# Kernel optimization log

Hardware: AMD Instinct MI355X
Metric: run time of the kernel (lower is better)

## Reference

```python
import jax, jax.numpy as jnp
import numpy as np

N_NODES = 100000
N_EDGES = 1600000
N_FEAT = 64
HIDDEN = 64
N_GRAPHS = 64
N_CLASSES = 2


def setup_inputs() -> dict:
    key = jax.random.key(0)
    ks = jax.random.split(key, 12)
    x = jax.random.normal(ks[0], (N_NODES, N_FEAT), dtype=jnp.float32)
    edge_index = jax.random.randint(ks[1], (2, N_EDGES), 0, N_NODES, dtype=jnp.int32)
    batch = jnp.sort(jax.random.randint(ks[2], (N_NODES,), 0, N_GRAPHS, dtype=jnp.int32))
    # Glorot-style init for GCNConv weights, zeros for biases (PyG default)
    def glorot(k, fan_in, fan_out):
        s = jnp.sqrt(6.0 / (fan_in + fan_out))
        return jax.random.uniform(k, (fan_in, fan_out), jnp.float32, -s, s)
    W1 = glorot(ks[3], N_FEAT, HIDDEN); b1 = jnp.zeros((HIDDEN,), jnp.float32)
    W2 = glorot(ks[4], HIDDEN, HIDDEN); b2 = jnp.zeros((HIDDEN,), jnp.float32)
    W3 = glorot(ks[5], HIDDEN, HIDDEN); b3 = jnp.zeros((HIDDEN,), jnp.float32)
    Wl = glorot(ks[6], HIDDEN, N_CLASSES); bl = jnp.zeros((N_CLASSES,), jnp.float32)
    return {"x": x, "edge_index": edge_index, "batch": batch,
            "W1": W1, "b1": b1, "W2": W2, "b2": b2, "W3": W3, "b3": b3,
            "Wl": Wl, "bl": bl}


def _gcn_conv(h, W, b, src, dst, dinv, n_nodes):
    # GCNConv with self-loops: out_i = sum_j d_i^-1/2 d_j^-1/2 (x_j W) + d_i^-1 (x_i W) + b
    h = h @ W                                   # [N, H]
    coef = (dinv[src] * dinv[dst])[:, None]     # [E, 1]
    agg = jax.ops.segment_sum(coef * h[src], dst, num_segments=n_nodes)
    return agg + (dinv * dinv)[:, None] * h + b


def reference(x, edge_index, batch, W1, b1, W2, b2, W3, b3, Wl, bl):
    src, dst = edge_index[0], edge_index[1]
    # degree of A + I (edge weight 1), shared by all three convs
    deg = jax.ops.segment_sum(jnp.ones((N_EDGES,), x.dtype), dst, num_segments=N_NODES) + 1.0
    dinv = jax.lax.rsqrt(deg)

    h = jax.nn.relu(_gcn_conv(x, W1, b1, src, dst, dinv, N_NODES))
    h = jax.nn.relu(_gcn_conv(h, W2, b2, src, dst, dinv, N_NODES))
    h = _gcn_conv(h, W3, b3, src, dst, dinv, N_NODES)

    # global_mean_pool over graph ids
    sums = jax.ops.segment_sum(h, batch, num_segments=N_GRAPHS)
    cnts = jax.ops.segment_sum(jnp.ones((N_NODES,), x.dtype), batch, num_segments=N_GRAPHS)
    pooled = sums / jnp.maximum(cnts, 1.0)[:, None]

    # dropout(p=0.5) is identity in eval mode
    return pooled @ Wl + bl
```

## Files before the change

### kernel.cpp

```cpp
#include <hip/hip_runtime.h>


#define NF 64
#define ELLW 64
#define BINSHIFT 9
#define BINW 512
#define NB 196
#define BINCAP 9216
#define LPITCH 68

typedef __attribute__((ext_vector_type(8))) _Float16 f16x8;
typedef __attribute__((ext_vector_type(4))) _Float16 f16x4;
typedef __attribute__((ext_vector_type(4))) float f32x4;

__device__ inline unsigned short f2h_u(float f) {
    return __builtin_bit_cast(unsigned short, (_Float16)f);
}
__device__ inline unsigned int pack_h2(float a, float b) {
    unsigned int ua = f2h_u(a), ub = f2h_u(b);
    return ua | (ub << 16);
}

__global__ void binA_kernel(const int* __restrict__ src, const int* __restrict__ dst,
                            int* __restrict__ binCnt, int* __restrict__ binEdges,
                            int nE, int chunk) {
    __shared__ int hist[NB];
    __shared__ int base[NB];
    int t = threadIdx.x;
    if (t < NB) hist[t] = 0;
    __syncthreads();
    int e0 = blockIdx.x * chunk;
    int e1 = min(e0 + chunk, nE);
    for (int e = e0 + t; e < e1; e += blockDim.x) {
        int b = dst[e] >> BINSHIFT;
        atomicAdd(&hist[b], 1);
    }
    __syncthreads();
    if (t < NB) {
        base[t] = atomicAdd(&binCnt[t], hist[t]);
        hist[t] = 0;
    }
    __syncthreads();
    for (int e = e0 + t; e < e1; e += blockDim.x) {
        int d = dst[e];
        int b = d >> BINSHIFT;
        int pos = base[b] + atomicAdd(&hist[b], 1);
        if (pos < BINCAP)
            binEdges[(size_t)b * BINCAP + pos] = src[e] | ((d & (BINW - 1)) << 17);
    }
}

__global__ void __launch_bounds__(512) binB_kernel(const int* __restrict__ binEdges,
                            const int* __restrict__ binCnt, int* __restrict__ cnt,
                            float* __restrict__ dinv, int* __restrict__ colELL, int n,
                            unsigned int* __restrict__ dummyA, unsigned int* __restrict__ dummyB) {
    __shared__ int lcnt[BINW];
    int t = threadIdx.x;
    int b = blockIdx.x;
    if (b == 0 && t < 32) { dummyA[t] = 0u; dummyB[t] = 0u; }
    for (int i = t; i < BINW; i += blockDim.x) lcnt[i] = 1;
    __syncthreads();
    int m = binCnt[b];
    if (m > BINCAP) m = BINCAP;
    const int* be = binEdges + (size_t)b * BINCAP;
    int nbase = b << BINSHIFT;
    for (int e = t; e < m; e += blockDim.x) {
        int v = be[e];
        int s = v & 0x1FFFF;
        int dl = v >> 17;
        int pos = atomicAdd(&lcnt[dl], 1);
        if (pos < ELLW) colELL[(size_t)(nbase + dl) * ELLW + pos] = s;
    }
    __syncthreads();
    for (int i = t; i < BINW; i += blockDim.x) {
        int node = nbase + i;
        if (node < n) {
            int c = lcnt[i];
            if (c > ELLW) c = ELLW;
            colELL[(size_t)node * ELLW + 0] = node;
            int cpad = (c + 3) & ~3;
            for (int j = c; j < cpad; ++j)
                colELL[(size_t)node * ELLW + j] = n;
            cnt[node] = c;
            dinv[node] = rsqrtf((float)c);
        }
    }
}

__global__ void prep_kernel(const float* __restrict__ W1, const float* __restrict__ W2,
                            const float* __restrict__ W3, unsigned short* __restrict__ w1h,
                            unsigned short* __restrict__ w2h, unsigned short* __restrict__ w3h) {
    int t = blockIdx.x * blockDim.x + threadIdx.x;
    if (t < NF * NF) {
        w1h[t] = f2h_u(W1[t]);
        w2h[t] = f2h_u(W2[t]);
        w3h[t] = f2h_u(W3[t]);
    }
}

__device__ __forceinline__ void gather_row_mlp8(
        const unsigned short* __restrict__ hB, const int* __restrict__ cr,
        int cl4, int fq, float acc[8]) {
    int q = 0;
    for (; q + 8 <= cl4; q += 8) {
        int s0 = cr[q], s1 = cr[q + 1], s2 = cr[q + 2], s3 = cr[q + 3];
        int s4 = cr[q + 4], s5 = cr[q + 5], s6 = cr[q + 6], s7 = cr[q + 7];
        f16x8 h0 = *(const f16x8*)(hB + (size_t)s0 * NF + fq * 8);
        f16x8 h1 = *(const f16x8*)(hB + (size_t)s1 * NF + fq * 8);
        f16x8 h2 = *(const f16x8*)(hB + (size_t)s2 * NF + fq * 8);
        f16x8 h3 = *(const f16x8*)(hB + (size_t)s3 * NF + fq * 8);
        f16x8 h4 = *(const f16x8*)(hB + (size_t)s4 * NF + fq * 8);
        f16x8 h5 = *(const f16x8*)(hB + (size_t)s5 * NF + fq * 8);
        f16x8 h6 = *(const f16x8*)(hB + (size_t)s6 * NF + fq * 8);
        f16x8 h7 = *(const f16x8*)(hB + (size_t)s7 * NF + fq * 8);
        f16x8 ttA = (h0 + h1) + (h2 + h3);
        f16x8 ttB = (h4 + h5) + (h6 + h7);
#pragma unroll
        for (int j = 0; j < 8; ++j) acc[j] += (float)ttA[j];
#pragma unroll
        for (int j = 0; j < 8; ++j) acc[j] += (float)ttB[j];
    }
    if (q + 4 <= cl4) {
        int s0 = cr[q], s1 = cr[q + 1], s2 = cr[q + 2], s3 = cr[q + 3];
        f16x8 h0 = *(const f16x8*)(hB + (size_t)s0 * NF + fq * 8);
        f16x8 h1 = *(const f16x8*)(hB + (size_t)s1 * NF + fq * 8);
        f16x8 h2 = *(const f16x8*)(hB + (size_t)s2 * NF + fq * 8);
        f16x8 h3 = *(const f16x8*)(hB + (size_t)s3 * NF + fq * 8);
        f16x8 tt = (h0 + h1) + (h2 + h3);
#pragma unroll
        for (int j = 0; j < 8; ++j) acc[j] += (float)tt[j];
    }
}

__device__ inline void load_W_frags(const unsigned short* __restrict__ Wh, int r16, int kq,
                                    f16x8 bfr[4][2]) {
#pragma unroll
    for (int nt = 0; nt < 4; ++nt)
#pragma unroll
        for (int kh = 0; kh < 2; ++kh) {
            f16x8 f;
#pragma unroll
            for (int j = 0; j < 8; ++j)
                f[j] = __builtin_bit_cast(_Float16,
                        Wh[(kh * 32 + kq * 8 + j) * NF + nt * 16 + r16]);
            bfr[nt][kh] = f;
        }
}

__global__ void __launch_bounds__(256) gemm1_mfma_kernel(const float* __restrict__ A,
                                                         const unsigned short* __restrict__ Wh,
                                                         const float* __restrict__ dinv,
                                                         unsigned short* __restrict__ outB, int n) {
    __shared__ unsigned short T[4][16 * LPITCH];
    int lane = threadIdx.x & 63;
    int r16 = lane & 15, kq = lane >> 4;
    int wv = threadIdx.x >> 6;
    int wid = blockIdx.x * 4 + wv;
    int nw = gridDim.x * 4;
    f16x8 bfr[4][2];
    load_W_frags(Wh, r16, kq, bfr);
    int ntiles = n >> 4;
    for (int t = wid; t < ntiles; t += nw) {
        int r0 = t << 4;
        const float* ar = A + (size_t)(r0 + r16) * NF + kq * 8;
        f16x8 a0, a1;
        float4 v0 = *(const float4*)(ar);
        float4 v1 = *(const float4*)(ar + 4);
        float4 v2 = *(const float4*)(ar + 32);
        float4 v3 = *(const float4*)(ar + 36);
        a0[0] = (_Float16)v0.x; a0[1] = (_Float16)v0.y;
        a0[2] = (_Float16)v0.z; a0[3] = (_Float16)v0.w;
        a0[4] = (_Float16)v1.x; a0[5] = (_Float16)v1.y;
        a0[6] = (_Float16)v1.z; a0[7] = (_Float16)v1.w;
        a1[0] = (_Float16)v2.x; a1[1] = (_Float16)v2.y;
        a1[2] = (_Float16)v2.z; a1[3] = (_Float16)v2.w;
        a1[4] = (_Float16)v3.x; a1[5] = (_Float16)v3.y;
        a1[6] = (_Float16)v3.z; a1[7] = (_Float16)v3.w;
        f32x4 acc[4];
#pragma unroll
        for (int nt = 0; nt < 4; ++nt) {
            acc[nt] = (f32x4)(0.0f);
            acc[nt] = __builtin_amdgcn_mfma_f32_16x16x32_f16(a0, bfr[nt][0], acc[nt], 0, 0, 0);
            acc[nt] = __builtin_amdgcn_mfma_f32_16x16x32_f16(a1, bfr[nt][1], acc[nt], 0, 0, 0);
        }
        float ds[4];
#pragma unroll
        for (int reg = 0; reg < 4; ++reg) ds[reg] = dinv[r0 + kq * 4 + reg];
        unsigned short* Tw = T[wv];
#pragma unroll
        for (int nt = 0; nt < 4; ++nt)
#pragma unroll
            for (int reg = 0; reg < 4; ++reg)
                Tw[(kq * 4 + reg) * LPITCH + nt * 16 + r16] = f2h_u(acc[nt][reg] * ds[reg]);
#pragma unroll
        for (int it = 0; it < 4; ++it) {
            int row = it * 4 + kq;
            uint2 v = *(const uint2*)&Tw[row * LPITCH + r16 * 4];
            *(uint2*)(outB + (size_t)(r0 + row) * NF + r16 * 4) = v;
        }
    }
}

__global__ void __launch_bounds__(256) fused_agg_gemm_kernel(
        const unsigned short* __restrict__ hB, const int* __restrict__ colELL,
        const int* __restrict__ cnt, const float* __restrict__ dinv,
        const float* __restrict__ bias, const unsigned short* __restrict__ Wh,
        unsigned short* __restrict__ outB, int n) {
    __shared__ int Icol[32 * 32];
    __shared__ int Icnt[32];
    __shared__ unsigned short Tin[2][2048];
    __shared__ unsigned short Tout[2][16 * LPITCH];
    int t = threadIdx.x;
    int lane = t & 63;
    int wv = t >> 6;
    int es = lane >> 3;
    int fq = lane & 7;
    int r16 = lane & 15, kq = lane >> 4;
    int r0 = (int)(blockIdx.x << 5);
    {
        int srow = t >> 3, sj = t & 7;
        ((int4*)Icol)[t] = *(const int4*)(colELL + (size_t)(r0 + srow) * ELLW + sj * 4);
    }
    if (t < 32) Icnt[t] = cnt[r0 + t];
    int s0 = (wv & 1) << 1;
    f16x8 bfr[2][2];
#pragma unroll
    for (int si = 0; si < 2; ++si)
#pragma unroll
        for (int kh = 0; kh < 2; ++kh) {
            f16x8 f;
#pragma unroll
            for (int j = 0; j < 8; ++j)
                f[j] = __builtin_bit_cast(_Float16,
                        Wh[(kh * 32 + kq * 8 + j) * NF + (s0 + si) * 16 + r16]);
            bfr[si][kh] = f;
        }
    __syncthreads();
    int lrow = wv * 8 + es;
    int row = r0 + lrow;
    int c = Icnt[lrow];
    int cpad = (c + 3) & ~3;
    int cl4 = cpad < 32 ? cpad : 32;
    const int* cr = Icol + lrow * 32;
    float acc[8];
#pragma unroll
    for (int j = 0; j < 8; ++j) acc[j] = 0.f;
    gather_row_mlp8(hB, cr, cl4, fq, acc);
    if (c > 32) {
        const int* crg = colELL + (size_t)row * ELLW;
        for (int qq = 32; qq + 4 <= cpad; qq += 4) {
            int s0e = crg[qq], s1e = crg[qq + 1], s2e = crg[qq + 2], s3e = crg[qq + 3];
            f16x8 h0 = *(const f16x8*)(hB + (size_t)s0e * NF + fq * 8);
            f16x8 h1 = *(const f16x8*)(hB + (size_t)s1e * NF + fq * 8);
            f16x8 h2 = *(const f16x8*)(hB + (size_t)s2e * NF + fq * 8);
            f16x8 h3 = *(const f16x8*)(hB + (size_t)s3e * NF + fq * 8);
            f16x8 tt = (h0 + h1) + (h2 + h3);
#pragma unroll
            for (int j = 0; j < 8; ++j) acc[j] += (float)tt[j];
        }
    }
    {
        float dd = dinv[row];
        float4 bA = *(const float4*)(bias + fq * 8);
        float4 bB = *(const float4*)(bias + fq * 8 + 4);
        float r0f = fmaxf(dd * acc[0] + bA.x, 0.f), r1f = fmaxf(dd * acc[1] + bA.y, 0.f);
        float r2f = fmaxf(dd * acc[2] + bA.z, 0.f), r3f = fmaxf(dd * acc[3] + bA.w, 0.f);
        float r4f = fmaxf(dd * acc[4] + bB.x, 0.f), r5f = fmaxf(dd * acc[5] + bB.y, 0.f);
        float r6f = fmaxf(dd * acc[6] + bB.z, 0.f), r7f = fmaxf(dd * acc[7] + bB.w, 0.f);
        int4 v;
        v.x = (int)pack_h2(r0f, r1f);
        v.y = (int)pack_h2(r2f, r3f);
        v.z = (int)pack_h2(r4f, r5f);
        v.w = (int)pack_h2(r6f, r7f);
        int tile = lrow >> 4;
        int idx = ((fq >> 2) << 10) + (((fq & 3) * 16 + (lrow & 15)) << 3);
        *(int4*)&Tin[tile][idx] = v;
    }
    __syncthreads();
    int tile = wv >> 1;
    f16x8 A0 = *(const f16x8*)&Tin[tile][lane * 8];
    f16x8 A1 = *(const f16x8*)&Tin[tile][1024 + lane * 8];
    float ds[4];
#pragma unroll
    for (int reg = 0; reg < 4; ++reg) ds[reg] = dinv[r0 + tile * 16 + kq * 4 + reg];
#pragma unroll
    for (int si = 0; si < 2; ++si) {
        f32x4 accC = (f32x4)(0.0f);
        accC = __builtin_amdgcn_mfma_f32_16x16x32_f16(A0, bfr[si][0], accC, 0, 0, 0);
        accC = __builtin_amdgcn_mfma_f32_16x16x32_f16(A1, bfr[si][1], accC, 0, 0, 0);
#pragma unroll
        for (int reg = 0; reg < 4; ++reg)
            Tout[tile][(kq * 4 + reg) * LPITCH + (s0 + si) * 16 + r16] =
                f2h_u(accC[reg] * ds[reg]);
    }
    __syncthreads();
    {
        int orow = t >> 3, oc = t & 7;
        const unsigned short* p = &Tout[orow >> 4][(orow & 15) * LPITCH + oc * 8];
        uint2 v0 = *(const uint2*)(p);
        uint2 v1 = *(const uint2*)(p + 4);
        int4 v; v.x = (int)v0.x; v.y = (int)v0.y; v.z = (int)v1.x; v.w = (int)v1.y;
        *(int4*)(outB + (size_t)(r0 + orow) * NF + oc * 8) = v;
    }
}

__global__ void __launch_bounds__(256) gather3_pool_kernel(
        const unsigned short* __restrict__ hB, const int* __restrict__ colELL,
        const int* __restrict__ cnt, const float* __restrict__ dinv,
        const float* __restrict__ bias, const int* __restrict__ batch,
        float* __restrict__ pooled, int n) {
    __shared__ int Icol[32 * 32];
    __shared__ int Icnt[32];
    __shared__ int Ibatch[32];
    __shared__ float PL[2][NF];
    int t = threadIdx.x;
    int lane = t & 63;
    int wv = t >> 6;
    int es = lane >> 3;
    int fq = lane & 7;
    int r0 = (int)(blockIdx.x << 5);
    {
        int srow = t >> 3, sj = t & 7;
        ((int4*)Icol)[t] = *(const int4*)(colELL + (size_t)(r0 + srow) * ELLW + sj * 4);
    }
    if (t < 32) { Icnt[t] = cnt[r0 + t]; Ibatch[t] = batch[r0 + t]; }
    if (t >= 128) PL[(t - 128) >> 6][t & 63] = 0.f;
    __syncthreads();
    int lrow = wv * 8 + es;
    int row = r0 + lrow;
    int c = Icnt[lrow];
    int cpad = (c + 3) & ~3;
    int cl4 = cpad < 32 ? cpad : 32;
    const int* cr = Icol + lrow * 32;
    float acc[8];
#pragma unroll
    for (int j = 0; j < 8; ++j) acc[j] = 0.f;
    gather_row_mlp8(hB, cr, cl4, fq, acc);
    if (c > 32) {
        const int* crg = colELL + (size_t)row * ELLW;
        for (int qq = 32; qq + 4 <= cpad; qq += 4) {
            int s0 = crg[qq], s1 = crg[qq + 1], s2 = crg[qq + 2], s3 = crg[qq + 3];
            f16x8 h0 = *(const f16x8*)(hB + (size_t)s0 * NF + fq * 8);
            f16x8 h1 = *(const f16x8*)(hB + (size_t)s1 * NF + fq * 8);
            f16x8 h2 = *(const f16x8*)(hB + (size_t)s2 * NF + fq * 8);
            f16x8 h3 = *(const f16x8*)(hB + (size_t)s3 * NF + fq * 8);
            f16x8 tt = (h0 + h1) + (h2 + h3);
#pragma unroll
            for (int j = 0; j < 8; ++j) acc[j] += (float)tt[j];
        }
    }
    float dd = dinv[row];
    float4 bA = *(const float4*)(bias + fq * 8);
    float4 bB = *(const float4*)(bias + fq * 8 + 4);
    float r[8];
    r[0] = dd * acc[0] + bA.x; r[1] = dd * acc[1] + bA.y;
    r[2] = dd * acc[2] + bA.z; r[3] = dd * acc[3] + bA.w;
    r[4] = dd * acc[4] + bB.x; r[5] = dd * acc[5] + bB.y;
    r[6] = dd * acc[6] + bB.z; r[7] = dd * acc[7] + bB.w;
    int g = Ibatch[lrow];
    int gb = Ibatch[0];
    int sel = g - gb;
    unsigned long long one_graph = __ballot(sel == 0);
    if (one_graph == ~0ULL) {
#pragma unroll
        for (int j = 0; j < 8; ++j) {
            float v = r[j];
            v += __shfl_xor(v, 8);
            v += __shfl_xor(v, 16);
            v += __shfl_xor(v, 32);
            if (es == 0) atomicAdd(&PL[0][fq * 8 + j], v);
        }
    } else {
#pragma unroll
        for (int j = 0; j < 8; ++j) {
            float v0 = sel == 0 ? r[j] : 0.f;
            float v1 = sel == 1 ? r[j] : 0.f;
            v0 += __shfl_xor(v0, 8);  v1 += __shfl_xor(v1, 8);
            v0 += __shfl_xor(v0, 16); v1 += __shfl_xor(v1, 16);
            v0 += __shfl_xor(v0, 32); v1 += __shfl_xor(v1, 32);
            if (es == 0) {
                atomicAdd(&PL[0][fq * 8 + j], v0);
                atomicAdd(&PL[1][fq * 8 + j], v1);
            }
            if (sel >= 2)
                atomicAdd(&pooled[g * NF + fq * 8 + j], r[j]);
        }
    }
    __syncthreads();
    if (t < 128) {
        int s = t >> 6, f = t & 63;
        float v = PL[s][f];
        if (v != 0.f) atomicAdd(&pooled[(gb + s) * NF + f], v);
    }
}

__global__ void counts_kernel(const int* __restrict__ batch, float* __restrict__ counts, int n) {
    __shared__ int h[64];
    int t = threadIdx.x;
    if (t < 64) h[t] = 0;
    __syncthreads();
    for (int i = blockIdx.x * blockDim.x + t; i < n; i += gridDim.x * blockDim.x)
        atomicAdd(&h[batch[i]], 1);
    __syncthreads();
    if (t < 64 && h[t] > 0) atomicAdd(&counts[t], (float)h[t]);
}

__global__ void final_kernel(const float* __restrict__ pooled, const float* __restrict__ counts,
                             const float* __restrict__ Wl, const float* __restrict__ bl,
                             float* __restrict__ out) {
    int t = threadIdx.x;
    int g = t >> 1, c = t & 1;
    float inv = 1.0f / fmaxf(counts[g], 1.0f);
    float s = 0.0f;
#pragma unroll
    for (int j = 0; j < NF; ++j) s += pooled[g * NF + j] * Wl[j * 2 + c];
    out[t] = s * inv + bl[c];
}

extern "C" void kernel_launch(void* const* d_in, const int* in_sizes, int n_in,
                              void* d_out, int out_size, void* d_ws, size_t ws_size,
                              hipStream_t stream) {
    const float* x     = (const float*)d_in[0];
    const int*   ei    = (const int*)d_in[1];
    const int*   batch = (const int*)d_in[2];
    const float* W1    = (const float*)d_in[3];
    const float* b1    = (const float*)d_in[4];
    const float* W2    = (const float*)d_in[5];
    const float* b2    = (const float*)d_in[6];
    const float* W3    = (const float*)d_in[7];
    const float* b3    = (const float*)d_in[8];
    const float* Wl    = (const float*)d_in[9];
    const float* bl    = (const float*)d_in[10];
    float* out = (float*)d_out;

    const int n  = in_sizes[0] / NF;
    const int nE = in_sizes[1] / 2;
    const int* src = ei;
    const int* dst = ei + nE;

    char* ws = (char*)d_ws;
    auto alloc = [&](size_t bytes) {
        char* p = ws;
        ws += (bytes + 255) & ~(size_t)255;
        return p;
    };
    unsigned short* bufA = (unsigned short*)alloc((size_t)(n + 16) * NF * 2);
    unsigned short* bufB = (unsigned short*)alloc((size_t)(n + 16) * NF * 2);
    float* scratch = (float*)alloc((size_t)n * NF * 4);
    int*   binEdges = (int*)scratch;
    int*   colELL = (int*)alloc((size_t)n * ELLW * 4);
    float* dinv   = (float*)alloc((size_t)(n + 16) * 4);
    int*   cnt    = (int*)alloc((size_t)n * 4);
    unsigned short* w1h = (unsigned short*)alloc((size_t)NF * NF * 2);
    unsigned short* w2h = (unsigned short*)alloc((size_t)NF * NF * 2);
    unsigned short* w3h = (unsigned short*)alloc((size_t)NF * NF * 2);
    char*  ztail  = ws;
    int*   binCnt = (int*)alloc(NB * 4);
    float* pooled = (float*)alloc(64 * NF * 4);
    float* counts = (float*)alloc(64 * 4);
    size_t zbytes = (size_t)(ws - ztail);

    (void)hipMemsetAsync(ztail, 0, zbytes, stream);

    const int chunk = 3200;
    binA_kernel<<<(nE + chunk - 1) / chunk, 256, 0, stream>>>(src, dst, binCnt, binEdges, nE, chunk);
    binB_kernel<<<NB, 512, 0, stream>>>(binEdges, binCnt, cnt, dinv, colELL, n,
                                        (unsigned int*)(bufA + (size_t)n * NF),
                                        (unsigned int*)(bufB + (size_t)n * NF));
    counts_kernel<<<98, 1024, 0, stream>>>(batch, counts, n);
    prep_kernel<<<16, 256, 0, stream>>>(W1, W2, W3, w1h, w2h, w3h);

    gemm1_mfma_kernel<<<1563, 256, 0, stream>>>(x, w1h, dinv, bufA, n);
    fused_agg_gemm_kernel<<<n >> 5, 256, 0, stream>>>(bufA, colELL, cnt, dinv, b1, w2h, bufB, n);
    fused_agg_gemm_kernel<<<n >> 5, 256, 0, stream>>>(bufB, colELL, cnt, dinv, b2, w3h, bufA, n);
    gather3_pool_kernel<<<n >> 5, 256, 0, stream>>>(bufA, colELL, cnt, dinv, b3,
                                                    batch, pooled, n);

    final_kernel<<<1, 128, 0, stream>>>(pooled, counts, Wl, bl, out);
}
```

Before: 229.9 us.

## Store layer-3 features in 16-column slabs and gather per slab for cache locality

The second fused aggregate+GEMM kernel now writes its output as four 16-feature slabs (each n+16 rows), with a zeroed padding row per slab. The final gather+pool kernel is restructured so each block handles 128 rows for a single slab, with block indices interleaved across the four slabs. The aim is a smaller working set per gather pass (32 bytes per node instead of 128), so random neighbour reads hit L2/MALL more often. In exchange, edge indices are read four times and pooling needs more atomics, and only 2 lanes cover each row's features.

```diff
diff --git a/kernel.cpp b/kernel.cpp
--- a/kernel.cpp
+++ b/kernel.cpp
@@ -205,7 +205,7 @@
         const unsigned short* __restrict__ hB, const int* __restrict__ colELL,
         const int* __restrict__ cnt, const float* __restrict__ dinv,
         const float* __restrict__ bias, const unsigned short* __restrict__ Wh,
-        unsigned short* __restrict__ outB, int n) {
+        unsigned short* __restrict__ outB, int n, int slabOut) {
     __shared__ int Icol[32 * 32];
     __shared__ int Icnt[32];
     __shared__ unsigned short Tin[2][2048];
@@ -217,6 +217,11 @@
     int fq = lane & 7;
     int r16 = lane & 15, kq = lane >> 4;
     int r0 = (int)(blockIdx.x << 5);
+    int n16 = n + 16;
+    if (slabOut && blockIdx.x == 0 && t < 32) {
+        int sl = t >> 3, jj = t & 7;
+        ((unsigned int*)(outB + ((size_t)sl * n16 + n) * 16))[jj] = 0u;
+    }
     {
         int srow = t >> 3, sj = t & 7;
         ((int4*)Icol)[t] = *(const int4*)(colELL + (size_t)(r0 + srow) * ELLW + sj * 4);
@@ -300,97 +305,160 @@
         uint2 v0 = *(const uint2*)(p);
         uint2 v1 = *(const uint2*)(p + 4);
         int4 v; v.x = (int)v0.x; v.y = (int)v0.y; v.z = (int)v1.x; v.w = (int)v1.y;
-        *(int4*)(outB + (size_t)(r0 + orow) * NF + oc * 8) = v;
+        if (slabOut) {
+            int sl = oc >> 1, half = oc & 1;
+            *(int4*)(outB + ((size_t)sl * n16 + (r0 + orow)) * 16 + half * 8) = v;
+        } else {
+            *(int4*)(outB + (size_t)(r0 + orow) * NF + oc * 8) = v;
+        }
     }
 }
 
 __global__ void __launch_bounds__(256) gather3_pool_kernel(
-        const unsigned short* __restrict__ hB, const int* __restrict__ colELL,
+        const unsigned short* __restrict__ hB3, const int* __restrict__ colELL,
         const int* __restrict__ cnt, const float* __restrict__ dinv,
         const float* __restrict__ bias, const int* __restrict__ batch,
         float* __restrict__ pooled, int n) {
-    __shared__ int Icol[32 * 32];
-    __shared__ int Icnt[32];
-    __shared__ int Ibatch[32];
-    __shared__ float PL[2][NF];
+    __shared__ int Icol[128 * 32];
+    __shared__ int Icnt[128];
+    __shared__ int Ibatch[128];
+    __shared__ float PL[2][16];
     int t = threadIdx.x;
     int lane = t & 63;
     int wv = t >> 6;
-    int es = lane >> 3;
-    int fq = lane & 7;
-    int r0 = (int)(blockIdx.x << 5);
-    {
-        int srow = t >> 3, sj = t & 7;
-        ((int4*)Icol)[t] = *(const int4*)(colELL + (size_t)(r0 + srow) * ELLW + sj * 4);
-    }
-    if (t < 32) { Icnt[t] = cnt[r0 + t]; Ibatch[t] = batch[r0 + t]; }
-    if (t >= 128) PL[(t - 128) >> 6][t & 63] = 0.f;
-    __syncthreads();
-    int lrow = wv * 8 + es;
+    int bid = (int)blockIdx.x;
+    int xr = bid & 7;
+    int s = xr >> 1, sub = xr & 1;
+    int chunk = (bid >> 3) * 2 + sub;
+    int nchunks = (n + 127) >> 7;
+    if (chunk >= nchunks) return;
+    int r0 = chunk << 7;
+    int n16 = n + 16;
+    for (int i = t; i < 1024; i += 256) {
+        int srow = i >> 3, sj = i & 7;
+        int grow = r0 + srow;
+        int rr = grow < n ? grow : n - 1;
+        ((int4*)Icol)[i] = *(const int4*)(colELL + (size_t)rr * ELLW + sj * 4);
+    }
+    if (t < 128) {
+        int grow = r0 + t;
+        Icnt[t] = grow < n ? cnt[grow] : 0;
+        Ibatch[t] = grow < n ? batch[grow] : -1;
+    }
+    if (t < 32) ((float*)PL)[t] = 0.f;
+    __syncthreads();
+    int es = lane >> 1;
+    int fq = lane & 1;
+    int lrow = wv * 32 + es;
     int row = r0 + lrow;
-    int c = Icnt[lrow];
+    bool valid = row < n;
+    int c = valid ? Icnt[lrow] : 0;
     int cpad = (c + 3) & ~3;
     int cl4 = cpad < 32 ? cpad : 32;
     const int* cr = Icol + lrow * 32;
+    const unsigned short* hs = hB3 + (size_t)s * n16 * 16;
     float acc[8];
 #pragma unroll
     for (int j = 0; j < 8; ++j) acc[j] = 0.f;
-    gather_row_mlp8(hB, cr, cl4, fq, acc);
+    {
+        int q = 0;
+        for (; q + 8 <= cl4; q += 8) {
+            int s0 = cr[q], s1 = cr[q + 1], s2 = cr[q + 2], s3 = cr[q + 3];
+            int s4 = cr[q + 4], s5 = cr[q + 5], s6 = cr[q + 6], s7 = cr[q + 7];
+            f16x8 h0 = *(const f16x8*)(hs + (size_t)s0 * 16 + fq * 8);
+            f16x8 h1 = *(const f16x8*)(hs + (size_t)s1 * 16 + fq * 8);
+            f16x8 h2 = *(const f16x8*)(hs + (size_t)s2 * 16 + fq * 8);
+            f16x8 h3 = *(const f16x8*)(hs + (size_t)s3 * 16 + fq * 8);
+            f16x8 h4 = *(const f16x8*)(hs + (size_t)s4 * 16 + fq * 8);
+            f16x8 h5 = *(const f16x8*)(hs + (size_t)s5 * 16 + fq * 8);
+            f16x8 h6 = *(const f16x8*)(hs + (size_t)s6 * 16 + fq * 8);
+            f16x8 h7 = *(const f16x8*)(hs + (size_t)s7 * 16 + fq * 8);
+            f16x8 ttA = (h0 + h1) + (h2 + h3);
+            f16x8 ttB = (h4 + h5) + (h6 + h7);
+#pragma unroll
+            for (int j = 0; j < 8; ++j) acc[j] += (float)ttA[j];
+#pragma unroll
+            for (int j = 0; j < 8; ++j) acc[j] += (float)ttB[j];
+        }
+        if (q + 4 <= cl4) {
+            int s0 = cr[q], s1 = cr[q + 1], s2 = cr[q + 2], s3 = cr[q + 3];
+            f16x8 h0 = *(const f16x8*)(hs + (size_t)s0 * 16 + fq * 8);
+            f16x8 h1 = *(const f16x8*)(hs + (size_t)s1 * 16 + fq * 8);
+            f16x8 h2 = *(const f16x8*)(hs + (size_t)s2 * 16 + fq * 8);
+            f16x8 h3 = *(const f16x8*)(hs + (size_t)s3 * 16 + fq * 8);
+            f16x8 tt = (h0 + h1) + (h2 + h3);
+#pragma unroll
+            for (int j = 0; j < 8; ++j) acc[j] += (float)tt[j];
+        }
+    }
     if (c > 32) {
         const int* crg = colELL + (size_t)row * ELLW;
         for (int qq = 32; qq + 4 <= cpad; qq += 4) {
-            int s0 = crg[qq], s1 = crg[qq + 1], s2 = crg[qq + 2], s3 = crg[qq + 3];
-            f16x8 h0 = *(const f16x8*)(hB + (size_t)s0 * NF + fq * 8);
-            f16x8 h1 = *(const f16x8*)(hB + (size_t)s1 * NF + fq * 8);
-            f16x8 h2 = *(const f16x8*)(hB + (size_t)s2 * NF + fq * 8);
-            f16x8 h3 = *(const f16x8*)(hB + (size_t)s3 * NF + fq * 8);
+            int s0e = crg[qq], s1e = crg[qq + 1], s2e = crg[qq + 2], s3e = crg[qq + 3];
+            f16x8 h0 = *(const f16x8*)(hs + (size_t)s0e * 16 + fq * 8);
+            f16x8 h1 = *(const f16x8*)(hs + (size_t)s1e * 16 + fq * 8);
+            f16x8 h2 = *(const f16x8*)(hs + (size_t)s2e * 16 + fq * 8);
+            f16x8 h3 = *(const f16x8*)(hs + (size_t)s3e * 16 + fq * 8);
             f16x8 tt = (h0 + h1) + (h2 + h3);
 #pragma unroll
             for (int j = 0; j < 8; ++j) acc[j] += (float)tt[j];
         }
     }
-    float dd = dinv[row];
-    float4 bA = *(const float4*)(bias + fq * 8);
-    float4 bB = *(const float4*)(bias + fq * 8 + 4);
     float r[8];
-    r[0] = dd * acc[0] + bA.x; r[1] = dd * acc[1] + bA.y;
-    r[2] = dd * acc[2] + bA.z; r[3] = dd * acc[3] + bA.w;
-    r[4] = dd * acc[4] + bB.x; r[5] = dd * acc[5] + bB.y;
-    r[6] = dd * acc[6] + bB.z; r[7] = dd * acc[7] + bB.w;
-    int g = Ibatch[lrow];
-    int gb = Ibatch[0];
-    int sel = g - gb;
-    unsigned long long one_graph = __ballot(sel == 0);
-    if (one_graph == ~0ULL) {
-#pragma unroll
-        for (int j = 0; j < 8; ++j) {
-            float v = r[j];
-            v += __shfl_xor(v, 8);
-            v += __shfl_xor(v, 16);
-            v += __shfl_xor(v, 32);
-            if (es == 0) atomicAdd(&PL[0][fq * 8 + j], v);
-        }
-    } else {
-#pragma unroll
-        for (int j = 0; j < 8; ++j) {
-            float v0 = sel == 0 ? r[j] : 0.f;
-            float v1 = sel == 1 ? r[j] : 0.f;
-            v0 += __shfl_xor(v0, 8);  v1 += __shfl_xor(v1, 8);
-            v0 += __shfl_xor(v0, 16); v1 += __shfl_xor(v1, 16);
-            v0 += __shfl_xor(v0, 32); v1 += __shfl_xor(v1, 32);
-            if (es == 0) {
-                atomicAdd(&PL[0][fq * 8 + j], v0);
-                atomicAdd(&PL[1][fq * 8 + j], v1);
+    {
+        float dd = valid ? dinv[row] : 0.f;
+        float4 bA = *(const float4*)(bias + s * 16 + fq * 8);
+        float4 bB = *(const float4*)(bias + s * 16 + fq * 8 + 4);
+        r[0] = valid ? dd * acc[0] + bA.x : 0.f;
+        r[1] = valid ? dd * acc[1] + bA.y : 0.f;
+        r[2] = valid ? dd * acc[2] + bA.z : 0.f;
+        r[3] = valid ? dd * acc[3] + bA.w : 0.f;
+        r[4] = valid ? dd * acc[4] + bB.x : 0.f;
+        r[5] = valid ? dd * acc[5] + bB.y : 0.f;
+        r[6] = valid ? dd * acc[6] + bB.z : 0.f;
+        r[7] = valid ? dd * acc[7] + bB.w : 0.f;
+    }
+    int gbB = Ibatch[0];
+    if (Ibatch[wv * 32] >= 0) {
+        int g = Ibatch[lrow];
+        int sel = g - gbB;
+        unsigned long long one = __ballot(sel == 0);
+        if (one == ~0ULL) {
+#pragma unroll
+            for (int j = 0; j < 8; ++j) {
+                float v = r[j];
+                v += __shfl_xor(v, 2);
+                v += __shfl_xor(v, 4);
+                v += __shfl_xor(v, 8);
+                v += __shfl_xor(v, 16);
+                v += __shfl_xor(v, 32);
+                if (es == 0) atomicAdd(&PL[0][fq * 8 + j], v);
             }
-            if (sel >= 2)
-                atomicAdd(&pooled[g * NF + fq * 8 + j], r[j]);
-        }
-    }
-    __syncthreads();
-    if (t < 128) {
-        int s = t >> 6, f = t & 63;
-        float v = PL[s][f];
-        if (v != 0.f) atomicAdd(&pooled[(gb + s) * NF + f], v);
+        } else {
+#pragma unroll
+            for (int j = 0; j < 8; ++j) {
+                float v0 = sel == 0 ? r[j] : 0.f;
+                float v1 = sel == 1 ? r[j] : 0.f;
+                v0 += __shfl_xor(v0, 2);  v1 += __shfl_xor(v1, 2);
+                v0 += __shfl_xor(v0, 4);  v1 += __shfl_xor(v1, 4);
+                v0 += __shfl_xor(v0, 8);  v1 += __shfl_xor(v1, 8);
+                v0 += __shfl_xor(v0, 16); v1 += __shfl_xor(v1, 16);
+                v0 += __shfl_xor(v0, 32); v1 += __shfl_xor(v1, 32);
+                if (es == 0) {
+                    atomicAdd(&PL[0][fq * 8 + j], v0);
+                    atomicAdd(&PL[1][fq * 8 + j], v1);
+                }
+                if (sel >= 2)
+                    atomicAdd(&pooled[g * NF + s * 16 + fq * 8 + j], r[j]);
+            }
+        }
+    }
+    __syncthreads();
+    if (t < 32) {
+        int sl = t >> 4, f = t & 15;
+        float v = PL[sl][f];
+        int gg = gbB + sl;
+        if (v != 0.f && gg < 64) atomicAdd(&pooled[gg * NF + s * 16 + f], v);
     }
 }
 
@@ -471,10 +539,14 @@
     prep_kernel<<<16, 256, 0, stream>>>(W1, W2, W3, w1h, w2h, w3h);
 
     gemm1_mfma_kernel<<<1563, 256, 0, stream>>>(x, w1h, dinv, bufA, n);
-    fused_agg_gemm_kernel<<<n >> 5, 256, 0, stream>>>(bufA, colELL, cnt, dinv, b1, w2h, bufB, n);
-    fused_agg_gemm_kernel<<<n >> 5, 256, 0, stream>>>(bufB, colELL, cnt, dinv, b2, w3h, bufA, n);
-    gather3_pool_kernel<<<n >> 5, 256, 0, stream>>>(bufA, colELL, cnt, dinv, b3,
-                                                    batch, pooled, n);
+    fused_agg_gemm_kernel<<<n >> 5, 256, 0, stream>>>(bufA, colELL, cnt, dinv, b1, w2h, bufB, n, 0);
+    fused_agg_gemm_kernel<<<n >> 5, 256, 0, stream>>>(bufB, colELL, cnt, dinv, b2, w3h, bufA, n, 1);
+    {
+        int nchunks = (n + 127) >> 7;
+        int grid = ((nchunks + 1) >> 1) * 8;
+        gather3_pool_kernel<<<grid, 256, 0, stream>>>(bufA, colELL, cnt, dinv, b3,
+                                                      batch, pooled, n);
+    }
 
     final_kernel<<<1, 128, 0, stream>>>(pooled, counts, Wl, bl, out);
 }
```

Measured after the change: 242.4 us. 5.4% more time.
